# Optimization experiments

Hardware: AMD Instinct MI355X
Metric: run time of the kernel (lower is better)

The kernel has to match this reference:

```python
import jax, jax.numpy as jnp
import numpy as np

INPUT_SIZE = 1024
HIDDEN_SIZE = 1024
BATCH = 8192


def setup_inputs() -> dict:
    key = jax.random.key(0)
    ks = jax.random.split(key, 14)
    stdv = 1.0 / HIDDEN_SIZE ** 0.5
    u = lambda k, shape: jax.random.uniform(k, shape, jnp.float32, -stdv, stdv)
    H, I = HIDDEN_SIZE, INPUT_SIZE
    return {
        "x": jax.random.normal(ks[0], (BATCH, I), jnp.float32),
        "hidden": jax.random.normal(ks[1], (BATCH, H), jnp.float32),
        "weight_xr": u(ks[2], (H, I)),
        "weight_hr": u(ks[3], (H, H)),
        "bias_r": u(ks[4], (H,)),
        "weight_xz": u(ks[5], (H, I)),
        "weight_hz": u(ks[6], (H, H)),
        "bias_z": u(ks[7], (H,)),
        "weight_xh": u(ks[8], (H, I)),
        "weight_hh": u(ks[9], (H, H)),
        "bias_h": u(ks[10], (H,)),
        "weight_c": u(ks[11], (H, I + H)),
        "bias_c": u(ks[12], (H,)),
        "weight_hat_h": u(ks[13], (H, I + H)),
        "bias_hat_h": u(jax.random.fold_in(key, 99), (H,)),
    }


def reference(x, hidden, weight_xr, weight_hr, bias_r, weight_xz, weight_hz, bias_z,
              weight_xh, weight_hh, bias_h, weight_c, bias_c, weight_hat_h, bias_hat_h):
    # combined: [B, I+H]
    combined = jnp.concatenate([x, hidden], axis=1)
    c_t = combined @ weight_c.T + bias_c                      # [B, H]
    a_t = jax.nn.softmax(c_t, axis=1)
    hat_h_t = a_t * jax.nn.relu(combined @ weight_hat_h.T + bias_hat_h)
    r_t = jax.nn.sigmoid(x @ weight_xr.T + bias_r + hidden @ weight_hr.T)
    z_t = jax.nn.sigmoid(x @ weight_xz.T + bias_z + hidden @ weight_hz.T)
    h_tilde = jnp.tanh(x @ weight_xh.T + bias_h + (r_t * hidden) @ weight_hh.T)
    h_t = (1.0 - z_t) * h_tilde + z_t * hidden + hat_h_t
    return h_t
```

## Files before the change

### kernel.cpp

```cpp
#include <hip/hip_runtime.h>

typedef unsigned short ushort_t;
typedef __attribute__((ext_vector_type(8))) short short8;
typedef __attribute__((ext_vector_type(4))) float float4v;
typedef __attribute__((ext_vector_type(4))) ushort_t ushort4v;

#define B_ROWS 8192
#define HDIM   1024
#define GLD    5120

__device__ __forceinline__ float bf2f(ushort_t u) {
    return __uint_as_float(((unsigned)u) << 16);
}
__device__ __forceinline__ ushort_t f2bf(float f) {
    unsigned u = __float_as_uint(f);
    u += 0x7FFFu + ((u >> 16) & 1u);
    return (ushort_t)(u >> 16);
}

__global__ __launch_bounds__(256) void pack_all(
    const float* __restrict__ x, const float* __restrict__ h,
    const float* __restrict__ wc, const float* __restrict__ what,
    const float* __restrict__ wxr, const float* __restrict__ whr,
    const float* __restrict__ wxz, const float* __restrict__ whz,
    const float* __restrict__ wxh, const float* __restrict__ whh,
    ushort_t* __restrict__ A, ushort_t* __restrict__ W,
    ushort_t* __restrict__ Whh)
{
    const int bid = blockIdx.x;
    float4v v;
    ushort_t* dst;
    size_t i4;
    if (bid < 16384) {
        i4 = ((size_t)bid * 256 + threadIdx.x) * 4;
        int c = (int)(i4 & 2047);
        size_t b = i4 >> 11;
        const float* src = (c < 1024) ? (x + b * 1024 + c)
                                      : (h + b * 1024 + (c - 1024));
        v = *(const float4v*)src;
        dst = A + i4;
    } else if (bid < 26624) {
        i4 = ((size_t)(bid - 16384) * 256 + threadIdx.x) * 4;
        int j = (int)(i4 >> 11);
        int k = (int)(i4 & 2047);
        int r = j >> 10, jr = j & 1023;
        if (r == 0) {
            v = *(const float4v*)(wc + (size_t)j * 2048 + k);
        } else if (r == 1) {
            v = *(const float4v*)(what + (size_t)jr * 2048 + k);
        } else if (r == 4) {
            v = (k < 1024) ? *(const float4v*)(wxh + (size_t)jr * 1024 + k)
                           : (float4v){0.f, 0.f, 0.f, 0.f};
        } else {
            const float* p0 = (r == 2) ? wxr : wxz;
            const float* p1 = (r == 2) ? whr : whz;
            const float* p = (k < 1024) ? (p0 + (size_t)jr * 1024 + k)
                                        : (p1 + (size_t)jr * 1024 + (k - 1024));
            v = *(const float4v*)p;
        }
        dst = W + i4;
    } else {
        i4 = ((size_t)(bid - 26624) * 256 + threadIdx.x) * 4;
        v = *(const float4v*)(whh + i4);
        dst = Whh + i4;
    }
    ushort4v o;
#pragma unroll
    for (int t = 0; t < 4; ++t) o[t] = f2bf(v[t]);
    *(ushort4v*)dst = o;
}


#define GLOAD(gp, lp) __builtin_amdgcn_global_load_lds( \
    (const __attribute__((address_space(1))) void*)(gp), \
    (__attribute__((address_space(3))) void*)(lp), 16, 0, 0)

#define BARRIER do { __builtin_amdgcn_s_barrier(); \
    __builtin_amdgcn_sched_barrier(0); } while (0)
#define WLG do { \
    asm volatile("s_waitcnt lgkmcnt(0)" ::: "memory"); \
    __builtin_amdgcn_sched_barrier(0); } while (0)
#define WVM6 do { \
    asm volatile("s_waitcnt vmcnt(6)" ::: "memory"); \
    __builtin_amdgcn_sched_barrier(0); } while (0)
#define WVM4 do { \
    asm volatile("s_waitcnt vmcnt(4)" ::: "memory"); \
    __builtin_amdgcn_sched_barrier(0); } while (0)
#define WVM2 do { \
    asm volatile("s_waitcnt vmcnt(2)" ::: "memory"); \
    __builtin_amdgcn_sched_barrier(0); } while (0)
#define WVM0 do { \
    asm volatile("s_waitcnt vmcnt(0)" ::: "memory"); \
    __builtin_amdgcn_sched_barrier(0); } while (0)

#define STAGE_A(S, H, KT) do { \
    GLOAD(A + (aO0 + (H) * 262144u + (unsigned)(KT) * 64u), dstA + (S) * 32768 + (H) * 8192); \
    GLOAD(A + (aO1 + (H) * 262144u + (unsigned)(KT) * 64u), dstA + (S) * 32768 + (H) * 8192 + 512); } while (0)
#define STAGE_B(S, H, KT) do { \
    GLOAD(B + (bO0 + (H) * 262144u + (unsigned)(KT) * 64u), dstB + (S) * 32768 + (H) * 8192); \
    GLOAD(B + (bO1 + (H) * 262144u + (unsigned)(KT) * 64u), dstB + (S) * 32768 + (H) * 8192 + 512); } while (0)

#define RD_A(BK, S, H) do { \
    _Pragma("unroll") \
    for (int mi = 0; mi < 4; ++mi) { \
        BK[mi]     = *(const short8*)(lds + (S) * 32768 + (H) * 8192 + mi * 1024 + Ard0); \
        BK[4 + mi] = *(const short8*)(lds + (S) * 32768 + (H) * 8192 + mi * 1024 + Ard1); } } while (0)

#define RD_A_KH(BK, S, H, KH) do { \
    _Pragma("unroll") \
    for (int mi = 0; mi < 4; ++mi) \
        BK[(KH) * 4 + mi] = *(const short8*)(lds + (S) * 32768 + (H) * 8192 + mi * 1024 + ((KH) ? Ard1 : Ard0)); } while (0)

#define RD_B(BK, S, H) do { \
    _Pragma("unroll") \
    for (int ni = 0; ni < 2; ++ni) { \
        BK[ni]     = *(const short8*)(lds + (S) * 32768 + 16384 + (H) * 8192 + ni * 1024 + Brd0); \
        BK[2 + ni] = *(const short8*)(lds + (S) * 32768 + 16384 + (H) * 8192 + ni * 1024 + Brd1); } } while (0)

#define MM(HA, HB, AB, BB) do { \
    __builtin_amdgcn_s_setprio(1); \
    _Pragma("unroll") \
    for (int mi = 0; mi < 4; ++mi) { \
        _Pragma("unroll") \
        for (int ni = 0; ni < 2; ++ni) { \
            acc[HA][HB][mi][ni] = __builtin_amdgcn_mfma_f32_16x16x32_bf16( \
                AB[mi], BB[ni], acc[HA][HB][mi][ni], 0, 0, 0); \
            acc[HA][HB][mi][ni] = __builtin_amdgcn_mfma_f32_16x16x32_bf16( \
                AB[4 + mi], BB[2 + ni], acc[HA][HB][mi][ni], 0, 0, 0); } } \
    __builtin_amdgcn_s_setprio(0); } while (0)

__global__ __launch_bounds__(512, 2) void gemm1(
    const ushort_t* __restrict__ A, const ushort_t* __restrict__ B,
    ushort_t* __restrict__ C)
{
    const int bid = blockIdx.x;
    int bx, by;
    if (bid < 512) { int hI = (bid & 7) * 64 + (bid >> 3); by = hI >> 4; bx = hI & 15; }
    else           { int b = bid - 512; int lI = (b & 7) * 16 + (b >> 3); by = lI >> 2; bx = 16 + (lI & 3); }
    const int bn0 = bx * 256;
    const int bm0 = by * 256;
    const int K = (bx >= 16) ? 1024 : 2048;
    const int NIT = K >> 7;

    __shared__ ushort_t lds[65536];

    const int t = threadIdx.x;
    const int w = t >> 6, lane = t & 63;
    const int q = lane >> 4, r16 = lane & 15;

    const int c0 = ((q ^ (r16 & 7)) << 3);
    const int c1 = (((4 + q) ^ (r16 & 7)) << 3);
    const int Ard0 = ((w >> 2) * 64 + r16) * 64 + c0;
    const int Ard1 = ((w >> 2) * 64 + r16) * 64 + c1;
    const int Brd0 = ((w & 3) * 32 + r16) * 64 + c0;
    const int Brd1 = ((w & 3) * 32 + r16) * 64 + c1;

    const unsigned srow0 = (unsigned)(w * 16 + ((lane >> 3) & 7));
    const unsigned kcO = (unsigned)(((lane & 7) ^ (lane >> 3)) << 3);
    const unsigned aO0 = ((unsigned)bm0 + srow0) * 2048u + kcO;
    const unsigned aO1 = aO0 + 8u * 2048u;
    const unsigned bO0 = ((unsigned)bn0 + srow0) * 2048u + kcO;
    const unsigned bO1 = bO0 + 8u * 2048u;
    ushort_t* dstA = lds + w * 1024;
    ushort_t* dstB = lds + 16384 + w * 1024;

    float4v acc[2][2][4][2];
#pragma unroll
    for (int i = 0; i < 2; ++i)
#pragma unroll
        for (int j = 0; j < 2; ++j)
#pragma unroll
            for (int m = 0; m < 4; ++m)
#pragma unroll
                for (int n = 0; n < 2; ++n)
                    acc[i][j][m][n] = {0.f, 0.f, 0.f, 0.f};

    short8 fX[8], fY[8];
    short8 gA[4], gB[4];

    STAGE_A(0, 0, 0);
    STAGE_B(0, 1, 0);
    STAGE_B(0, 0, 0);
    STAGE_A(0, 1, 0);
    STAGE_A(1, 0, 1);
    STAGE_B(1, 1, 1);
    WVM4;
    BARRIER;
    RD_A(fX, 0, 0);
    RD_B(gA, 0, 0);

#pragma unroll 1
    for (int it = 0; it < NIT - 1; ++it) {
        const int kO  = 2 * it + 1;
        const int kE2 = 2 * it + 2;
        const int kO2 = 2 * it + 3;
        WLG; BARRIER;
        STAGE_B(1, 0, kO);
        RD_B(gB, 0, 1);
        MM(0, 0, fX, gA);
        WVM6; WLG; BARRIER;
        STAGE_A(1, 1, kO);
        RD_A(fY, 0, 1);
        MM(0, 1, fX, gB);
        WVM6; WLG; BARRIER;
        STAGE_A(0, 0, kE2);
        RD_A_KH(fX, 1, 0, 0);
        MM(1, 1, fY, gB);
        WVM4; WLG; BARRIER;
        STAGE_B(0, 1, kE2);
        RD_A_KH(fX, 1, 0, 1);
        RD_B(gB, 1, 0);
        MM(1, 0, fY, gA);
        WLG; BARRIER;
        STAGE_B(0, 0, kE2);
        RD_B(gA, 1, 1);
        MM(0, 0, fX, gB);
        WVM6; WLG; BARRIER;
        STAGE_A(0, 1, kE2);
        RD_A(fY, 1, 1);
        MM(0, 1, fX, gA);
        WVM6; WLG; BARRIER;
        STAGE_A(1, 0, kO2);
        RD_A_KH(fX, 0, 0, 0);
        MM(1, 1, fY, gA);
        WVM4; WLG; BARRIER;
        STAGE_B(1, 1, kO2);
        RD_A_KH(fX, 0, 0, 1);
        RD_B(gA, 0, 0);
        MM(1, 0, fY, gB);
    }

    {
        const int kO = 2 * (NIT - 1) + 1;
        WLG; BARRIER;
        STAGE_B(1, 0, kO);
        RD_B(gB, 0, 1);
        MM(0, 0, fX, gA);
        WVM6; WLG; BARRIER;
        STAGE_A(1, 1, kO);
        RD_A(fY, 0, 1);
        MM(0, 1, fX, gB);
        WVM6; WLG; BARRIER;
        RD_A_KH(fX, 1, 0, 0);
        MM(1, 1, fY, gB);
        WVM2; WLG; BARRIER;
        RD_A_KH(fX, 1, 0, 1);
        RD_B(gB, 1, 0);
        MM(1, 0, fY, gA);
        WLG; BARRIER;
        RD_B(gA, 1, 1);
        MM(0, 0, fX, gB);
        WVM0; WLG; BARRIER;
        RD_A(fY, 1, 1);
        MM(0, 1, fX, gA);
        WLG; BARRIER;
        MM(1, 1, fY, gA);
        WLG; BARRIER;
        MM(1, 0, fY, gB);
    }

    {
        const int wm2 = w >> 2, wn2 = w & 3;
#pragma unroll
        for (int ha = 0; ha < 2; ++ha)
#pragma unroll
            for (int hb = 0; hb < 2; ++hb)
#pragma unroll
                for (int mi = 0; mi < 4; ++mi)
#pragma unroll
                    for (int ni = 0; ni < 2; ++ni)
#pragma unroll
                        for (int reg = 0; reg < 4; ++reg) {
                            int row = bm0 + ha * 128 + wm2 * 64 + mi * 16 + q * 4 + reg;
                            int col = bn0 + hb * 128 + wn2 * 32 + ni * 16 + r16;
                            C[(size_t)row * GLD + col] = f2bf(acc[ha][hb][mi][ni][reg]);
                        }
    }
}

__global__ __launch_bounds__(256) void row_pass(
    ushort_t* __restrict__ G, const float* __restrict__ bias_c,
    const float* __restrict__ bias_hat, const float* __restrict__ bias_r,
    const float* __restrict__ hidden, ushort_t* __restrict__ rh)
{
    const int wave = threadIdx.x >> 6, lane = threadIdx.x & 63;
    const size_t row = (size_t)blockIdx.x * 4 + wave;
    ushort_t* g = G + row * GLD;
    const int c0 = lane * 16;

    float cv[16];
    {
        short8 a = *(const short8*)(g + c0);
        short8 b = *(const short8*)(g + c0 + 8);
#pragma unroll
        for (int i = 0; i < 8; ++i) {
            cv[i]     = bf2f((ushort_t)a[i]) + bias_c[c0 + i];
            cv[8 + i] = bf2f((ushort_t)b[i]) + bias_c[c0 + 8 + i];
        }
    }
    float mx = cv[0];
#pragma unroll
    for (int i = 1; i < 16; ++i) mx = fmaxf(mx, cv[i]);
#pragma unroll
    for (int m = 1; m < 64; m <<= 1) mx = fmaxf(mx, __shfl_xor(mx, m));
    float sum = 0.f;
#pragma unroll
    for (int i = 0; i < 16; ++i) { cv[i] = __expf(cv[i] - mx); sum += cv[i]; }
#pragma unroll
    for (int m = 1; m < 64; m <<= 1) sum += __shfl_xor(sum, m);
    const float inv = 1.0f / sum;

    {
        short8 a = *(const short8*)(g + 1024 + c0);
        short8 b = *(const short8*)(g + 1024 + c0 + 8);
        short8 oa, ob;
#pragma unroll
        for (int i = 0; i < 8; ++i) {
            float ha = bf2f((ushort_t)a[i]) + bias_hat[c0 + i];
            float hb = bf2f((ushort_t)b[i]) + bias_hat[c0 + 8 + i];
            oa[i] = (short)f2bf(cv[i] * inv * fmaxf(ha, 0.f));
            ob[i] = (short)f2bf(cv[8 + i] * inv * fmaxf(hb, 0.f));
        }
        *(short8*)(g + c0) = oa;
        *(short8*)(g + c0 + 8) = ob;
    }

    {
        short8 a = *(const short8*)(g + 2048 + c0);
        short8 b = *(const short8*)(g + 2048 + c0 + 8);
        const float* hp = hidden + row * 1024 + c0;
        short8 oa, ob;
#pragma unroll
        for (int i = 0; i < 8; ++i) {
            float ra = 1.0f / (1.0f + __expf(-(bf2f((ushort_t)a[i]) + bias_r[c0 + i])));
            float rb = 1.0f / (1.0f + __expf(-(bf2f((ushort_t)b[i]) + bias_r[c0 + 8 + i])));
            oa[i] = (short)f2bf(ra * hp[i]);
            ob[i] = (short)f2bf(rb * hp[8 + i]);
        }
        ushort_t* rp = rh + row * 1024 + c0;
        *(short8*)rp = oa;
        *(short8*)(rp + 8) = ob;
    }
}

#define CSTRIDE 132
__global__ __launch_bounds__(256) void gemm2_final(
    const ushort_t* __restrict__ A, const ushort_t* __restrict__ B,
    const ushort_t* __restrict__ G, const float* __restrict__ bias_z,
    const float* __restrict__ bias_h, const float* __restrict__ hidden,
    float* __restrict__ out)
{
    const int bn0 = blockIdx.x * 128;
    const int bm0 = blockIdx.y * 64;

    __shared__ ushort_t smem[64 * CSTRIDE];
    ushort_t* As = smem;
    ushort_t* Bs = smem + 2048;

    const int t = threadIdx.x;
    const int wave = t >> 6, lane = t & 63;
    const int wr = wave >> 1, wcq = wave & 1;
    const int q = lane >> 4, r16 = lane & 15;
    const int lrow = lane >> 2;
    const int lcol = (lane & 3) * 8;

    float4v acc[2][4];
#pragma unroll
    for (int i = 0; i < 2; ++i)
#pragma unroll
        for (int j = 0; j < 4; ++j)
            acc[i][j] = {0.f, 0.f, 0.f, 0.f};

    for (int k0 = 0; k0 < 1024; k0 += 32) {
#pragma unroll
        for (int j = 0; j < 3; ++j) {
            int l = wave * 3 + j;
            if (l < 4) {
                const ushort_t* gp = A + (size_t)(bm0 + l * 16 + lrow) * 1024 + k0 + lcol;
                __builtin_amdgcn_global_load_lds(
                    (const __attribute__((address_space(1))) void*)gp,
                    (__attribute__((address_space(3))) void*)(As + l * 512),
                    16, 0, 0);
            } else {
                const ushort_t* gp = B + (size_t)(bn0 + (l - 4) * 16 + lrow) * 1024 + k0 + lcol;
                __builtin_amdgcn_global_load_lds(
                    (const __attribute__((address_space(1))) void*)gp,
                    (__attribute__((address_space(3))) void*)(Bs + (l - 4) * 512),
                    16, 0, 0);
            }
        }
        __syncthreads();

        short8 af[2], bf[4];
#pragma unroll
        for (int mi = 0; mi < 2; ++mi)
            af[mi] = *(const short8*)&As[(wr * 32 + mi * 16 + r16) * 32 + q * 8];
#pragma unroll
        for (int ni = 0; ni < 4; ++ni)
            bf[ni] = *(const short8*)&Bs[(wcq * 64 + ni * 16 + r16) * 32 + q * 8];
#pragma unroll
        for (int mi = 0; mi < 2; ++mi)
#pragma unroll
            for (int ni = 0; ni < 4; ++ni)
                acc[mi][ni] = __builtin_amdgcn_mfma_f32_16x16x32_bf16(
                    af[mi], bf[ni], acc[mi][ni], 0, 0, 0);
        __syncthreads();
    }

#pragma unroll
    for (int mi = 0; mi < 2; ++mi)
#pragma unroll
        for (int ni = 0; ni < 4; ++ni)
#pragma unroll
            for (int reg = 0; reg < 4; ++reg) {
                int rl = wr * 32 + mi * 16 + q * 4 + reg;
                int cl = wcq * 64 + ni * 16 + r16;
                smem[rl * CSTRIDE + cl] = f2bf(acc[mi][ni][reg]);
            }
    __syncthreads();

    const int colL = t & 127;
    const int gc = bn0 + colL;
    const float bz = bias_z[gc];
    const float bh = bias_h[gc];
    const int rbase = t >> 7;
#pragma unroll 4
    for (int pass = 0; pass < 32; ++pass) {
        const int rowL = pass * 2 + rbase;
        const size_t gr = (size_t)(bm0 + rowL);
        const ushort_t* grow = G + gr * GLD;
        float z = 1.0f / (1.0f + __expf(-(bf2f(grow[3072 + gc]) + bz)));
        float targ = bf2f(grow[4096 + gc]) + bh + bf2f(smem[rowL * CSTRIDE + colL]);
        float th = 1.0f - 2.0f / (__expf(2.0f * targ) + 1.0f);
        out[gr * 1024 + gc] =
            (1.0f - z) * th + z * hidden[gr * 1024 + gc] + bf2f(grow[gc]);
    }
}


extern "C" void kernel_launch(void* const* d_in, const int* in_sizes, int n_in,
                              void* d_out, int out_size, void* d_ws, size_t ws_size,
                              hipStream_t stream)
{
    const float* x        = (const float*)d_in[0];
    const float* hidden   = (const float*)d_in[1];
    const float* wxr      = (const float*)d_in[2];
    const float* whr      = (const float*)d_in[3];
    const float* bias_r   = (const float*)d_in[4];
    const float* wxz      = (const float*)d_in[5];
    const float* whz      = (const float*)d_in[6];
    const float* bias_z   = (const float*)d_in[7];
    const float* wxh      = (const float*)d_in[8];
    const float* whh      = (const float*)d_in[9];
    const float* bias_h   = (const float*)d_in[10];
    const float* wc       = (const float*)d_in[11];
    const float* bias_c   = (const float*)d_in[12];
    const float* what     = (const float*)d_in[13];
    const float* bias_hat = (const float*)d_in[14];
    float* out = (float*)d_out;

    char* ws = (char*)d_ws;
    ushort_t* G     = (ushort_t*)(ws);
    ushort_t* Abf   = (ushort_t*)(ws + 83886080);
    ushort_t* Wbf   = (ushort_t*)(ws + 117440512);
    ushort_t* Whhbf = (ushort_t*)(ws + 138412032);
    ushort_t* rhbf  = (ushort_t*)(ws + 140509184);

    pack_all<<<27648, 256, 0, stream>>>(x, hidden, wc, what, wxr, whr, wxz, whz,
                                        wxh, whh, Abf, Wbf, Whhbf);

    gemm1<<<640, 512, 0, stream>>>(Abf, Wbf, G);

    row_pass<<<B_ROWS / 4, 256, 0, stream>>>(G, bias_c, bias_hat, bias_r, hidden, rhbf);

    gemm2_final<<<dim3(8, 128), 256, 0, stream>>>(rhbf, Whhbf, G, bias_z, bias_h,
                                                  hidden, out);
}
```

Baseline: 406.3 us.

## Restructure GEMM main loop into finer half-K sub-steps with smaller register fragments

Rewrites the software pipeline of the fused GEMM so that each barrier-separated step issues 8 MFMAs on half-K fragments (4 A, 2 B registers) instead of 16 on full-K fragments. LDS reads are moved after the MFMA cluster of each step, and global-to-LDS staging is rescheduled with new vmcnt thresholds. The aim is to reduce fragment register pressure and interleave LDS reads with MFMA work more finely. The cost is twice as many barriers per iteration, which may add synchronisation overhead.

```diff
diff --git a/kernel.cpp b/kernel.cpp
--- a/kernel.cpp
+++ b/kernel.cpp
@@ -80,53 +80,41 @@
 #define WLG do { \
     asm volatile("s_waitcnt lgkmcnt(0)" ::: "memory"); \
     __builtin_amdgcn_sched_barrier(0); } while (0)
-#define WVM6 do { \
-    asm volatile("s_waitcnt vmcnt(6)" ::: "memory"); \
+#define WVM(N) do { \
+    asm volatile("s_waitcnt vmcnt(" #N ")" ::: "memory"); \
     __builtin_amdgcn_sched_barrier(0); } while (0)
-#define WVM4 do { \
-    asm volatile("s_waitcnt vmcnt(4)" ::: "memory"); \
-    __builtin_amdgcn_sched_barrier(0); } while (0)
-#define WVM2 do { \
-    asm volatile("s_waitcnt vmcnt(2)" ::: "memory"); \
-    __builtin_amdgcn_sched_barrier(0); } while (0)
-#define WVM0 do { \
-    asm volatile("s_waitcnt vmcnt(0)" ::: "memory"); \
-    __builtin_amdgcn_sched_barrier(0); } while (0)
 
 #define STAGE_A(S, H, KT) do { \
-    GLOAD(A + (aO0 + (H) * 262144u + (unsigned)(KT) * 64u), dstA + (S) * 32768 + (H) * 8192); \
-    GLOAD(A + (aO1 + (H) * 262144u + (unsigned)(KT) * 64u), dstA + (S) * 32768 + (H) * 8192 + 512); } while (0)
+    GLOAD(A + (aO0 + (H) * 262144u + (unsigned)(KT) * 64u), \
+          dstA + (S) * 32768 + (H) * 8192); \
+    GLOAD(A + (aO0 + 16384u + (H) * 262144u + (unsigned)(KT) * 64u), \
+          dstA + (S) * 32768 + (H) * 8192 + 512); } while (0)
 #define STAGE_B(S, H, KT) do { \
-    GLOAD(B + (bO0 + (H) * 262144u + (unsigned)(KT) * 64u), dstB + (S) * 32768 + (H) * 8192); \
-    GLOAD(B + (bO1 + (H) * 262144u + (unsigned)(KT) * 64u), dstB + (S) * 32768 + (H) * 8192 + 512); } while (0)
-
-#define RD_A(BK, S, H) do { \
-    _Pragma("unroll") \
-    for (int mi = 0; mi < 4; ++mi) { \
-        BK[mi]     = *(const short8*)(lds + (S) * 32768 + (H) * 8192 + mi * 1024 + Ard0); \
-        BK[4 + mi] = *(const short8*)(lds + (S) * 32768 + (H) * 8192 + mi * 1024 + Ard1); } } while (0)
-
-#define RD_A_KH(BK, S, H, KH) do { \
+    GLOAD(B + (bO0 + (H) * 262144u + (unsigned)(KT) * 64u), \
+          dstB + (S) * 32768 + (H) * 8192); \
+    GLOAD(B + (bO0 + 16384u + (H) * 262144u + (unsigned)(KT) * 64u), \
+          dstB + (S) * 32768 + (H) * 8192 + 512); } while (0)
+
+#define RD_A4(BK, S, H, KH) do { \
     _Pragma("unroll") \
     for (int mi = 0; mi < 4; ++mi) \
-        BK[(KH) * 4 + mi] = *(const short8*)(lds + (S) * 32768 + (H) * 8192 + mi * 1024 + ((KH) ? Ard1 : Ard0)); } while (0)
-
-#define RD_B(BK, S, H) do { \
+        BK[mi] = *(const short8*)(lds + (S) * 32768 + (H) * 8192 + mi * 1024 \
+                                  + ((KH) ? Ard1 : Ard0)); } while (0)
+
+#define RD_B2(BK, S, H, KH) do { \
     _Pragma("unroll") \
-    for (int ni = 0; ni < 2; ++ni) { \
-        BK[ni]     = *(const short8*)(lds + (S) * 32768 + 16384 + (H) * 8192 + ni * 1024 + Brd0); \
-        BK[2 + ni] = *(const short8*)(lds + (S) * 32768 + 16384 + (H) * 8192 + ni * 1024 + Brd1); } } while (0)
-
-#define MM(HA, HB, AB, BB) do { \
+    for (int ni = 0; ni < 2; ++ni) \
+        BK[ni] = *(const short8*)(lds + 16384 + (S) * 32768 + (H) * 8192 + ni * 1024 \
+                                  + ((KH) ? Brd1 : Brd0)); } while (0)
+
+#define MM8(HA, HB, AB, BB) do { \
     __builtin_amdgcn_s_setprio(1); \
     _Pragma("unroll") \
     for (int mi = 0; mi < 4; ++mi) { \
         _Pragma("unroll") \
-        for (int ni = 0; ni < 2; ++ni) { \
+        for (int ni = 0; ni < 2; ++ni) \
             acc[HA][HB][mi][ni] = __builtin_amdgcn_mfma_f32_16x16x32_bf16( \
-                AB[mi], BB[ni], acc[HA][HB][mi][ni], 0, 0, 0); \
-            acc[HA][HB][mi][ni] = __builtin_amdgcn_mfma_f32_16x16x32_bf16( \
-                AB[4 + mi], BB[2 + ni], acc[HA][HB][mi][ni], 0, 0, 0); } } \
+                AB[mi], BB[ni], acc[HA][HB][mi][ni], 0, 0, 0); } \
     __builtin_amdgcn_s_setprio(0); } while (0)
 
 __global__ __launch_bounds__(512, 2) void gemm1(
@@ -158,9 +146,7 @@
     const unsigned srow0 = (unsigned)(w * 16 + ((lane >> 3) & 7));
     const unsigned kcO = (unsigned)(((lane & 7) ^ (lane >> 3)) << 3);
     const unsigned aO0 = ((unsigned)bm0 + srow0) * 2048u + kcO;
-    const unsigned aO1 = aO0 + 8u * 2048u;
     const unsigned bO0 = ((unsigned)bn0 + srow0) * 2048u + kcO;
-    const unsigned bO1 = bO0 + 8u * 2048u;
     ushort_t* dstA = lds + w * 1024;
     ushort_t* dstB = lds + 16384 + w * 1024;
 
@@ -175,88 +161,132 @@
                 for (int n = 0; n < 2; ++n)
                     acc[i][j][m][n] = {0.f, 0.f, 0.f, 0.f};
 
-    short8 fX[8], fY[8];
-    short8 gA[4], gB[4];
+    short8 X[4], Y[4];
+    short8 U[2], V[2];
 
     STAGE_A(0, 0, 0);
+    STAGE_B(0, 0, 0);
     STAGE_B(0, 1, 0);
-    STAGE_B(0, 0, 0);
     STAGE_A(0, 1, 0);
-    STAGE_A(1, 0, 1);
-    STAGE_B(1, 1, 1);
-    WVM4;
+    WVM(4);
     BARRIER;
-    RD_A(fX, 0, 0);
-    RD_B(gA, 0, 0);
+    RD_A4(X, 0, 0, 0);
+    RD_B2(U, 0, 0, 0);
 
 #pragma unroll 1
     for (int it = 0; it < NIT - 1; ++it) {
         const int kO  = 2 * it + 1;
         const int kE2 = 2 * it + 2;
-        const int kO2 = 2 * it + 3;
-        WLG; BARRIER;
+        WVM(2); WLG; BARRIER;
+        STAGE_A(1, 0, kO);
+        MM8(0, 0, X, U);
+        RD_B2(V, 0, 1, 0);
+        WVM(2); WLG; BARRIER;
         STAGE_B(1, 0, kO);
-        RD_B(gB, 0, 1);
-        MM(0, 0, fX, gA);
-        WVM6; WLG; BARRIER;
+        MM8(0, 1, X, V);
+        RD_A4(Y, 0, 1, 0);
+        WLG; BARRIER;
+        STAGE_B(1, 1, kO);
+        MM8(1, 1, Y, V);
+        RD_A4(X, 0, 0, 1);
+        WLG; BARRIER;
         STAGE_A(1, 1, kO);
-        RD_A(fY, 0, 1);
-        MM(0, 1, fX, gB);
-        WVM6; WLG; BARRIER;
+        MM8(1, 0, Y, U);
+        RD_B2(U, 0, 0, 1);
+        WLG; BARRIER;
         STAGE_A(0, 0, kE2);
-        RD_A_KH(fX, 1, 0, 0);
-        MM(1, 1, fY, gB);
-        WVM4; WLG; BARRIER;
+        MM8(0, 0, X, U);
+        RD_B2(V, 0, 1, 1);
+        WLG; BARRIER;
+        STAGE_B(0, 0, kE2);
+        MM8(0, 1, X, V);
+        RD_A4(Y, 0, 1, 1);
+        WVM(10); WLG; BARRIER;
         STAGE_B(0, 1, kE2);
-        RD_A_KH(fX, 1, 0, 1);
-        RD_B(gB, 1, 0);
-        MM(1, 0, fY, gA);
-        WLG; BARRIER;
-        STAGE_B(0, 0, kE2);
-        RD_B(gA, 1, 1);
-        MM(0, 0, fX, gB);
-        WVM6; WLG; BARRIER;
+        MM8(1, 1, Y, V);
+        RD_A4(X, 1, 0, 0);
+        WVM(10); WLG; BARRIER;
         STAGE_A(0, 1, kE2);
-        RD_A(fY, 1, 1);
-        MM(0, 1, fX, gA);
-        WVM6; WLG; BARRIER;
-        STAGE_A(1, 0, kO2);
-        RD_A_KH(fX, 0, 0, 0);
-        MM(1, 1, fY, gA);
-        WVM4; WLG; BARRIER;
-        STAGE_B(1, 1, kO2);
-        RD_A_KH(fX, 0, 0, 1);
-        RD_B(gA, 0, 0);
-        MM(1, 0, fY, gB);
+        MM8(1, 0, Y, U);
+        RD_B2(U, 1, 0, 0);
+        WVM(10); WLG; BARRIER;
+        MM8(0, 0, X, U);
+        RD_B2(V, 1, 1, 0);
+        WVM(8); WLG; BARRIER;
+        MM8(0, 1, X, V);
+        RD_A4(Y, 1, 1, 0);
+        WLG; BARRIER;
+        MM8(1, 1, Y, V);
+        RD_A4(X, 1, 0, 1);
+        WLG; BARRIER;
+        MM8(1, 0, Y, U);
+        RD_B2(U, 1, 0, 1);
+        WLG; BARRIER;
+        MM8(0, 0, X, U);
+        RD_B2(V, 1, 1, 1);
+        WLG; BARRIER;
+        MM8(0, 1, X, V);
+        RD_A4(Y, 1, 1, 1);
+        WVM(6); WLG; BARRIER;
+        MM8(1, 1, Y, V);
+        RD_A4(X, 0, 0, 0);
+        WVM(4); WLG; BARRIER;
+        MM8(1, 0, Y, U);
+        RD_B2(U, 0, 0, 0);
     }
 
     {
         const int kO = 2 * (NIT - 1) + 1;
-        WLG; BARRIER;
+        WVM(2); WLG; BARRIER;
+        STAGE_A(1, 0, kO);
+        MM8(0, 0, X, U);
+        RD_B2(V, 0, 1, 0);
+        WVM(2); WLG; BARRIER;
         STAGE_B(1, 0, kO);
-        RD_B(gB, 0, 1);
-        MM(0, 0, fX, gA);
-        WVM6; WLG; BARRIER;
+        MM8(0, 1, X, V);
+        RD_A4(Y, 0, 1, 0);
+        WLG; BARRIER;
+        STAGE_B(1, 1, kO);
+        MM8(1, 1, Y, V);
+        RD_A4(X, 0, 0, 1);
+        WLG; BARRIER;
         STAGE_A(1, 1, kO);
-        RD_A(fY, 0, 1);
-        MM(0, 1, fX, gB);
-        WVM6; WLG; BARRIER;
-        RD_A_KH(fX, 1, 0, 0);
-        MM(1, 1, fY, gB);
-        WVM2; WLG; BARRIER;
-        RD_A_KH(fX, 1, 0, 1);
-        RD_B(gB, 1, 0);
-        MM(1, 0, fY, gA);
-        WLG; BARRIER;
-        RD_B(gA, 1, 1);
-        MM(0, 0, fX, gB);
-        WVM0; WLG; BARRIER;
-        RD_A(fY, 1, 1);
-        MM(0, 1, fX, gA);
-        WLG; BARRIER;
-        MM(1, 1, fY, gA);
-        WLG; BARRIER;
-        MM(1, 0, fY, gB);
+        MM8(1, 0, Y, U);
+        RD_B2(U, 0, 0, 1);
+        WLG; BARRIER;
+        MM8(0, 0, X, U);
+        RD_B2(V, 0, 1, 1);
+        WLG; BARRIER;
+        MM8(0, 1, X, V);
+        RD_A4(Y, 0, 1, 1);
+        WVM(6); WLG; BARRIER;
+        MM8(1, 1, Y, V);
+        RD_A4(X, 1, 0, 0);
+        WVM(4); WLG; BARRIER;
+        MM8(1, 0, Y, U);
+        RD_B2(U, 1, 0, 0);
+        WVM(2); WLG; BARRIER;
+        MM8(0, 0, X, U);
+        RD_B2(V, 1, 1, 0);
+        WVM(0); WLG; BARRIER;
+        MM8(0, 1, X, V);
+        RD_A4(Y, 1, 1, 0);
+        WLG; BARRIER;
+        MM8(1, 1, Y, V);
+        RD_A4(X, 1, 0, 1);
+        WLG; BARRIER;
+        MM8(1, 0, Y, U);
+        RD_B2(U, 1, 0, 1);
+        WLG; BARRIER;
+        MM8(0, 0, X, U);
+        RD_B2(V, 1, 1, 1);
+        WLG; BARRIER;
+        MM8(0, 1, X, V);
+        RD_A4(Y, 1, 1, 1);
+        WLG; BARRIER;
+        MM8(1, 1, Y, V);
+        WLG; BARRIER;
+        MM8(1, 0, Y, U);
     }
 
     {
```

Result: faster. 363.1 us (-10.6%).
